# Optimization experiments

Measured on AMD Instinct MI355X. Metric: run time of the kernel, lower is better.

The kernel has to match this reference:

```python
import jax, jax.numpy as jnp
import numpy as np

# Module constants (match init_kwargs / DCNv4 defaults)
N, C, H, W = 4, 256, 128, 128
G = 4                       # DCNv4 default group
KS = 3                      # kernel_size
K = KS * KS                 # 9 sampling points per group
Cg = C // G                 # channels per group
PAD_OFF = int(np.ceil(G * K * 3 / 8) * 8)  # 112, padded offset_mask dim
EPS = 1e-5                  # BatchNorm2d eps


def setup_inputs() -> dict:
    key = jax.random.key(0)
    ks = jax.random.split(key, 6)
    s = 0.05
    return {
        "x": jax.random.normal(ks[0], (N, C, H, W), jnp.float32),
        "conv_w": jax.random.normal(ks[1], (C, C, 1, 1), jnp.float32) * s,
        "bn1_gamma": jnp.ones((C,), jnp.float32),
        "bn1_beta": jnp.zeros((C,), jnp.float32),
        "bn1_mean": jnp.zeros((C,), jnp.float32),
        "bn1_var": jnp.ones((C,), jnp.float32),
        "value_w": jax.random.normal(ks[2], (C, C), jnp.float32) * s,
        "value_b": jnp.zeros((C,), jnp.float32),
        "offset_w": jax.random.normal(ks[3], (PAD_OFF, C), jnp.float32) * s,
        "offset_b": jnp.zeros((PAD_OFF,), jnp.float32),
        "out_w": jax.random.normal(ks[4], (C, C), jnp.float32) * s,
        "out_b": jnp.zeros((C,), jnp.float32),
        "bn2_gamma": jnp.ones((C,), jnp.float32),
        "bn2_beta": jnp.zeros((C,), jnp.float32),
        "bn2_mean": jnp.zeros((C,), jnp.float32),
        "bn2_var": jnp.ones((C,), jnp.float32),
    }


def _bilinear(v, lh, lw):
    """Bilinear sample v:(N,H,W,G,Cg) at float locs lh/lw:(N,H,W,G); zero outside."""
    n, h, w, g, c = v.shape
    h0 = jnp.floor(lh)
    w0 = jnp.floor(lw)
    dh = lh - h0
    dw = lw - w0
    h0i = h0.astype(jnp.int32)
    w0i = w0.astype(jnp.int32)
    vf = v.reshape(n, h * w, g, c)

    def gather(hh, ww):
        valid = (hh >= 0) & (hh < h) & (ww >= 0) & (ww < w)
        idx = jnp.clip(hh, 0, h - 1) * w + jnp.clip(ww, 0, w - 1)
        out = jnp.take_along_axis(vf, idx.reshape(n, h * w, g)[..., None], axis=1)
        return out.reshape(n, h, w, g, c) * valid[..., None].astype(v.dtype)

    w00 = (1 - dh) * (1 - dw)
    w01 = (1 - dh) * dw
    w10 = dh * (1 - dw)
    w11 = dh * dw
    return (gather(h0i, w0i) * w00[..., None]
            + gather(h0i, w0i + 1) * w01[..., None]
            + gather(h0i + 1, w0i) * w10[..., None]
            + gather(h0i + 1, w0i + 1) * w11[..., None])


def _bn(x_nchw, gamma, beta, mean, var):
    scale = (gamma / jnp.sqrt(var + EPS))[None, :, None, None]
    return x_nchw * scale + (beta - mean * gamma / jnp.sqrt(var + EPS))[None, :, None, None]


def reference(x, conv_w, bn1_gamma, bn1_beta, bn1_mean, bn1_var,
              value_w, value_b, offset_w, offset_b, out_w, out_b,
              bn2_gamma, bn2_beta, bn2_mean, bn2_var):
    n, _, h, w = x.shape
    # ---- Conv(c1,c2,k=1): 1x1 conv (no bias) + BN + SiLU ----
    y = jnp.einsum('nchw,oc->nohw', x, conv_w[:, :, 0, 0])
    y = jax.nn.silu(_bn(y, bn1_gamma, bn1_beta, bn1_mean, bn1_var))

    # ---- DCNv4 on (N, L, C) tokens ----
    t = y.transpose(0, 2, 3, 1)                      # (N,H,W,C)
    v = t @ value_w.T + value_b                      # value_proj
    om = t @ offset_w.T + offset_b                   # (N,H,W,112)
    om = om[..., : G * K * 3].reshape(n, h, w, G, K * 3)
    off = om[..., : 2 * K].reshape(n, h, w, G, K, 2) # (dx, dy) per point
    mask = om[..., 2 * K:]                           # (N,H,W,G,K), no softmax in v4
    v = v.reshape(n, h, w, G, Cg)

    hi = jnp.arange(h, dtype=jnp.float32)[None, :, None, None]
    wi = jnp.arange(w, dtype=jnp.float32)[None, None, :, None]
    out = jnp.zeros_like(v)
    for k in range(K):  # fixed small kernel loop (9 points)
        i, j = divmod(k, KS)
        lh = hi + (i - 1) + off[..., k, 1]           # stride=1, pad=1, dil=1
        lw = wi + (j - 1) + off[..., k, 0]           # offset_scale=1.0
        out = out + mask[..., k, None] * _bilinear(v, lh, lw)

    o = out.reshape(n, h, w, C) @ out_w.T + out_b    # output_proj
    o = o.transpose(0, 3, 1, 2)                      # back to NCHW

    # ---- final BN + SiLU ----
    return jax.nn.silu(_bn(o, bn2_gamma, bn2_beta, bn2_mean, bn2_var))
```

## Files before the change

### kernel.cpp

```cpp
#include <hip/hip_runtime.h>
#include <cstdint>

typedef unsigned short u16;
typedef unsigned int   u32;
typedef __attribute__((ext_vector_type(8))) __bf16 bf16x8;
typedef __attribute__((ext_vector_type(2))) float  f32x2;
typedef __attribute__((ext_vector_type(4))) float  f32x4;
typedef __attribute__((ext_vector_type(4))) u32    u32x4;

#define N_IMG 4
#define C_DIM 256
#define H_DIM 128
#define W_DIM 128
#define HW    (H_DIM * W_DIM)
#define M_TOT (N_IMG * HW)
#define CG    64
#define PADOFF 112
#define NCAT  368
#define EPSV  1e-5f

__device__ __forceinline__ u16 f2b(float f) {
  u32 u = __float_as_uint(f);
  u += 0x7fffu + ((u >> 16) & 1u);
  return (u16)(u >> 16);
}

__device__ __forceinline__ void async_cp16(const void* g, void* l) {
  __builtin_amdgcn_global_load_lds(
      (const __attribute__((address_space(1))) void*)g,
      (__attribute__((address_space(3))) void*)l, 16, 0, 0);
}

__global__ __launch_bounds__(256) void cast_all(
    const float* __restrict__ a0, u16* __restrict__ o0,
    const float* __restrict__ a1, u16* __restrict__ o1,
    const float* __restrict__ a2, u16* __restrict__ o2,
    const float* __restrict__ a3, u16* __restrict__ o3) {
  int i = blockIdx.x * 256 + threadIdx.x;
  const float* in; u16* out; int base;
  if (i < 16384)      { in = a0; out = o0; base = 0; }
  else if (i < 32768) { in = a1; out = o1; base = 16384; }
  else if (i < 39936) { in = a2; out = o2; base = 32768; }
  else                { in = a3; out = o3; base = 39936; }
  int j = i - base;
  f32x4 v = reinterpret_cast<const f32x4*>(in)[j];
  u32 lo = (u32)f2b(v[0]) | ((u32)f2b(v[1]) << 16);
  u32 hi = (u32)f2b(v[2]) | ((u32)f2b(v[3]) << 16);
  reinterpret_cast<u32*>(out)[2 * j]     = lo;
  reinterpret_cast<u32*>(out)[2 * j + 1] = hi;
}

__global__ __launch_bounds__(256, 2) void fused_proj(
    const float* __restrict__ X, const u16* __restrict__ Bc,
    const u16* __restrict__ Wcat,
    u16* __restrict__ Vv, float* __restrict__ Om,
    const float* __restrict__ vbias, const float* __restrict__ obias,
    const float* __restrict__ gamma, const float* __restrict__ beta,
    const float* __restrict__ mean, const float* __restrict__ var) {
  constexpr int BM = 128, BK = 32;
  __shared__ __align__(16) u16 T[BM * C_DIM];
  __shared__ __align__(16) u16 As[BM * BK];
  __shared__ __align__(16) u16 Bs[BM * BK];
  const int tid  = threadIdx.x;
  const int lane = tid & 63;
  const int wave = tid >> 6;
  const int quad = lane >> 4;
  const int l16  = lane & 15;
  const int bm = blockIdx.x * BM;
  const int wm = (wave & 1) * 64;
  const int wn = (wave >> 1) * 64;
  const int img = bm >> 14;
  const int hw0 = bm & (HW - 1);
  const int p2  = (tid & 63) * 2;
  const int hh  = tid >> 6;
  const float* xb = X + (size_t)img * C_DIM * HW + hw0 + p2;

  f32x4 acc0[4][4] = {};
  f32x4 acc1[4][4] = {};
  for (int ko = 0; ko < C_DIM; ko += BK) {
    float a0[8], a1[8];
#pragma unroll
    for (int j = 0; j < 8; ++j) {
      f32x2 fv = *reinterpret_cast<const f32x2*>(
          xb + (size_t)(ko + hh * 8 + j) * HW);
      a0[j] = fv.x; a1[j] = fv.y;
    }
    u32x4 w0, w1;
#pragma unroll
    for (int j = 0; j < 4; ++j) {
      w0[j] = (u32)f2b(a0[2 * j]) | ((u32)f2b(a0[2 * j + 1]) << 16);
      w1[j] = (u32)f2b(a1[2 * j]) | ((u32)f2b(a1[2 * j + 1]) << 16);
    }
    {
      u32x4* Ar = reinterpret_cast<u32x4*>(As);
      int sw = hh ^ ((p2 >> 1) & 3);
      Ar[p2 * 4 + sw]       = w0;
      Ar[(p2 + 1) * 4 + sw] = w1;
    }
#pragma unroll
    for (int it = 0; it < 2; ++it) {
      int chunk = it * 256 + tid;
      int r  = chunk >> 2;
      int kk = (chunk & 3) << 3;
      async_cp16(Bc + (size_t)r * C_DIM + (ko + kk),
                 Bs + (size_t)(it * 256 + wave * 64) * 8);
    }
    __syncthreads();
    const bf16x8* Apf = reinterpret_cast<const bf16x8*>(As);
    const bf16x8* Bpf = reinterpret_cast<const bf16x8*>(Bs);
    bf16x8 af[4];
#pragma unroll
    for (int mi = 0; mi < 4; ++mi) {
      int r = wm + mi * 16 + l16;
      af[mi] = Apf[r * 4 + (quad ^ ((r >> 1) & 3))];
    }
    {
      bf16x8 bfr[4];
#pragma unroll
      for (int ni = 0; ni < 4; ++ni)
        bfr[ni] = Bpf[(wn + ni * 16 + l16) * 4 + quad];
#pragma unroll
      for (int mi = 0; mi < 4; ++mi)
#pragma unroll
        for (int ni = 0; ni < 4; ++ni)
          acc0[mi][ni] = __builtin_amdgcn_mfma_f32_16x16x32_bf16(
              af[mi], bfr[ni], acc0[mi][ni], 0, 0, 0);
    }
    __syncthreads();
#pragma unroll
    for (int it = 0; it < 2; ++it) {
      int chunk = it * 256 + tid;
      int r  = chunk >> 2;
      int kk = (chunk & 3) << 3;
      async_cp16(Bc + (size_t)(128 + r) * C_DIM + (ko + kk),
                 Bs + (size_t)(it * 256 + wave * 64) * 8);
    }
    __syncthreads();
    {
      bf16x8 bfr[4];
#pragma unroll
      for (int ni = 0; ni < 4; ++ni)
        bfr[ni] = Bpf[(wn + ni * 16 + l16) * 4 + quad];
#pragma unroll
      for (int mi = 0; mi < 4; ++mi)
#pragma unroll
        for (int ni = 0; ni < 4; ++ni)
          acc1[mi][ni] = __builtin_amdgcn_mfma_f32_16x16x32_bf16(
              af[mi], bfr[ni], acc1[mi][ni], 0, 0, 0);
    }
    __syncthreads();
  }
  auto epi1 = [&](f32x4 (&acc)[4][4], int bn) {
#pragma unroll
    for (int ni = 0; ni < 4; ++ni) {
      int n = bn + wn + ni * 16 + l16;
      float sc = gamma[n] * rsqrtf(var[n] + EPSV);
      float sh = beta[n] - mean[n] * sc;
#pragma unroll
      for (int mi = 0; mi < 4; ++mi) {
        int row = wm + mi * 16 + quad * 4;
#pragma unroll
        for (int i = 0; i < 4; ++i) {
          float y = acc[mi][ni][i] * sc + sh;
          y = y / (1.f + __expf(-y));
          int rr = row + i;
          T[rr * C_DIM + (((n >> 3) ^ (rr & 15)) << 3) + (n & 7)] = f2b(y);
        }
      }
    }
  };
  epi1(acc0, 0);
  epi1(acc1, 128);
  __syncthreads();

  auto stage2 = [&](u16* buf, int n0, int ko) {
#pragma unroll
    for (int it = 0; it < 2; ++it) {
      int chunk = it * 256 + tid;
      int r  = chunk >> 2;
      int kk = (chunk & 3) << 3;
      int br = n0 + r; if (br >= NCAT) br = NCAT - 1;
      async_cp16(Wcat + (size_t)br * C_DIM + (ko + kk),
                 buf + (size_t)(it * 256 + wave * 64) * 8);
    }
  };
  for (int nc = 0; nc < 3; ++nc) {
    const int n0 = nc * 128;
    f32x4 acc[4][4] = {};
    stage2(As, n0, 0);
    for (int koi = 0; koi < 8; ++koi) {
      const u16* cur = (koi & 1) ? Bs : As;
      u16*       nxt = (koi & 1) ? As : Bs;
      if (koi < 7) {
        stage2(nxt, n0, (koi + 1) * BK);
        asm volatile("s_waitcnt vmcnt(2)" ::: "memory");
      } else {
        asm volatile("s_waitcnt vmcnt(0)" ::: "memory");
      }
      __builtin_amdgcn_sched_barrier(0);
      __builtin_amdgcn_s_barrier();
      __builtin_amdgcn_sched_barrier(0);
      const bf16x8* Bpf = reinterpret_cast<const bf16x8*>(cur);
      bf16x8 af[4], bfr[4];
#pragma unroll
      for (int mi = 0; mi < 4; ++mi) {
        int row = wm + mi * 16 + l16;
        int ch  = koi * 4 + quad;
        af[mi] = *reinterpret_cast<const bf16x8*>(
            &T[row * C_DIM + ((ch ^ (row & 15)) << 3)]);
      }
#pragma unroll
      for (int ni = 0; ni < 4; ++ni)
        bfr[ni] = Bpf[(wn + ni * 16 + l16) * 4 + quad];
#pragma unroll
      for (int mi = 0; mi < 4; ++mi)
#pragma unroll
        for (int ni = 0; ni < 4; ++ni)
          acc[mi][ni] = __builtin_amdgcn_mfma_f32_16x16x32_bf16(
              af[mi], bfr[ni], acc[mi][ni], 0, 0, 0);
      __builtin_amdgcn_sched_barrier(0);
      __builtin_amdgcn_s_barrier();
    }
#pragma unroll
    for (int ni = 0; ni < 4; ++ni) {
      int n = n0 + wn + ni * 16 + l16;
      if (n < C_DIM) {
        float sh = vbias[n];
#pragma unroll
        for (int mi = 0; mi < 4; ++mi) {
          int mrow = bm + wm + mi * 16 + quad * 4;
#pragma unroll
          for (int i = 0; i < 4; ++i)
            Vv[(size_t)(mrow + i) * C_DIM + n] = f2b(acc[mi][ni][i] + sh);
        }
      } else {
        int col = n - C_DIM;
        bool ok = col < PADOFF;
        float sh = ok ? obias[col] : 0.f;
#pragma unroll
        for (int mi = 0; mi < 4; ++mi) {
          int mrow = bm + wm + mi * 16 + quad * 4;
#pragma unroll
          for (int i = 0; i < 4; ++i)
            if (ok) Om[(size_t)(mrow + i) * PADOFF + col] = acc[mi][ni][i] + sh;
        }
      }
    }
  }
}

__global__ __launch_bounds__(256) void gemm_out(
    const u16* __restrict__ A, const u16* __restrict__ B,
    float* __restrict__ Cf,
    const float* __restrict__ bias,
    const float* __restrict__ gamma, const float* __restrict__ beta,
    const float* __restrict__ mean, const float* __restrict__ var) {
  constexpr int BM = 128, BK = 32;
  __shared__ __align__(16) u16 As[2][BM * BK];
  __shared__ __align__(16) u16 Bs[2][BM * BK];
  const int tid  = threadIdx.x;
  const int lane = tid & 63;
  const int wave = tid >> 6;
  const int quad = lane >> 4;
  const int l16  = lane & 15;
  const int bm = blockIdx.x * BM;
  const int bn = blockIdx.y * BM;
  const int wm = (wave & 1) * 64;
  const int wn = (wave >> 1) * 64;

  auto stage = [&](int buf, int ko) {
#pragma unroll
    for (int it = 0; it < 2; ++it) {
      int chunk = it * 256 + tid;
      int r  = chunk >> 2;
      int kk = (chunk & 3) << 3;
      async_cp16(A + (size_t)(bm + r) * C_DIM + (ko + kk),
                 &As[buf][(it * 256 + wave * 64) * 8]);
      async_cp16(B + (size_t)(bn + r) * C_DIM + (ko + kk),
                 &Bs[buf][(it * 256 + wave * 64) * 8]);
    }
  };

  f32x4 acc[4][4] = {};

  stage(0, 0);
  for (int t = 0; t < 8; ++t) {
    const int cur = t & 1;
    if (t < 7) {
      stage(cur ^ 1, (t + 1) * BK);
      asm volatile("s_waitcnt vmcnt(4)" ::: "memory");
    } else {
      asm volatile("s_waitcnt vmcnt(0)" ::: "memory");
    }
    __builtin_amdgcn_sched_barrier(0);
    __builtin_amdgcn_s_barrier();
    __builtin_amdgcn_sched_barrier(0);
    const bf16x8* Ap = reinterpret_cast<const bf16x8*>(As[cur]);
    const bf16x8* Bp = reinterpret_cast<const bf16x8*>(Bs[cur]);
    bf16x8 af[4], bfr[4];
#pragma unroll
    for (int mi = 0; mi < 4; ++mi) af[mi] = Ap[(wm + mi * 16 + l16) * 4 + quad];
#pragma unroll
    for (int ni = 0; ni < 4; ++ni) bfr[ni] = Bp[(wn + ni * 16 + l16) * 4 + quad];
#pragma unroll
    for (int mi = 0; mi < 4; ++mi)
#pragma unroll
      for (int ni = 0; ni < 4; ++ni)
        acc[mi][ni] = __builtin_amdgcn_mfma_f32_16x16x32_bf16(
            af[mi], bfr[ni], acc[mi][ni], 0, 0, 0);
    __builtin_amdgcn_sched_barrier(0);
    __builtin_amdgcn_s_barrier();
  }

#pragma unroll
  for (int ni = 0; ni < 4; ++ni) {
    int n = bn + wn + ni * 16 + l16;
    float sc = gamma[n] * rsqrtf(var[n] + EPSV);
    float sh = beta[n] - mean[n] * sc + bias[n] * sc;
#pragma unroll
    for (int mi = 0; mi < 4; ++mi) {
      int mrow = bm + wm + mi * 16 + quad * 4;
      int img = mrow >> 14;
      int hw  = mrow & (HW - 1);
      f32x4 y;
#pragma unroll
      for (int i = 0; i < 4; ++i) {
        float z = acc[mi][ni][i] * sc + sh;
        y[i] = z / (1.f + __expf(-z));
      }
      *reinterpret_cast<f32x4*>(
          Cf + (size_t)img * C_DIM * HW + (size_t)n * HW + hw) = y;
    }
  }
}

__global__ __launch_bounds__(256) void dcn_sample(
    const u16* __restrict__ v, const float* __restrict__ om,
    u16* __restrict__ outp) {
  __shared__ float sm[16 * PADOFF];
  const int tid = threadIdx.x;
  const int bid = blockIdx.x;
  const int cpx = gridDim.x >> 3;
  const int wg  = (bid & 7) * cpx + (bid >> 3);
  const int m0  = wg * 16;
  {
    const float* src = om + (size_t)m0 * PADOFF;
#pragma unroll
    for (int i = 0; i < 7; ++i) sm[tid + i * 256] = src[tid + i * 256];
  }
  __syncthreads();
  const int c4 = tid & 3;
  const int g  = (tid >> 2) & 3;
  const int pl = tid >> 4;
  const int m  = m0 + pl;
  const int n  = m >> 14;
  const int hw = m & (HW - 1);
  const int h = hw >> 7, w = hw & 127;
  const float* p = sm + pl * PADOFF + g * 27;
  const u16* vb = v + (size_t)n * HW * C_DIM + g * CG + c4 * 16;
  float acc[16] = {};
#pragma unroll
  for (int k = 0; k < 9; ++k) {
    const int di = k / 3 - 1, dj = k % 3 - 1;
    float ox = p[2 * k], oy = p[2 * k + 1], mk = p[18 + k];
    float lh = (float)(h + di) + oy;
    float lw = (float)(w + dj) + ox;
    float fh = floorf(lh), fw = floorf(lw);
    float dh = lh - fh, dw = lw - fw;
    int h0 = (int)fh, w0 = (int)fw;
    float wy0 = (1.f - dh) * mk, wy1 = dh * mk;
    float wx0 = 1.f - dw, wx1 = dw;
    bool okw0 = (u32)w0 < (u32)W_DIM;
    bool okw1 = (u32)(w0 + 1) < (u32)W_DIM;
    int w0c = min(max(w0, 0), W_DIM - 1);
    int w1c = min(max(w0 + 1, 0), W_DIM - 1);
#pragma unroll
    for (int cy = 0; cy < 2; ++cy) {
      int hh = h0 + cy;
      bool okh = (u32)hh < (u32)H_DIM;
      int hc = min(max(hh, 0), H_DIM - 1);
      const u16* rowp = vb + (size_t)(hc << 7) * C_DIM;
      const u16* qA = rowp + (size_t)w0c * C_DIM;
      const u16* qB = rowp + (size_t)w1c * C_DIM;
      u32x4 a0 = *reinterpret_cast<const u32x4*>(qA);
      u32x4 a1 = *reinterpret_cast<const u32x4*>(qA + 8);
      u32x4 b0 = *reinterpret_cast<const u32x4*>(qB);
      u32x4 b1 = *reinterpret_cast<const u32x4*>(qB + 8);
      float wyc = (cy == 0) ? wy0 : wy1;
      float wtA = (okh && okw0) ? wyc * wx0 : 0.f;
      float wtB = (okh && okw1) ? wyc * wx1 : 0.f;
      u32 wp;
      asm("v_cvt_pk_bf16_f32 %0, %1, %2" : "=v"(wp) : "v"(wtA), "v"(wtB));
#pragma unroll
      for (int j = 0; j < 4; ++j) {
        u32 lo0 = __builtin_amdgcn_perm(a0[j], b0[j], 0x01000504u);
        u32 hi0 = __builtin_amdgcn_perm(a0[j], b0[j], 0x03020706u);
        u32 lo1 = __builtin_amdgcn_perm(a1[j], b1[j], 0x01000504u);
        u32 hi1 = __builtin_amdgcn_perm(a1[j], b1[j], 0x03020706u);
        asm("v_dot2_f32_bf16 %0, %1, %2, %3"
            : "=v"(acc[2 * j]) : "v"(lo0), "v"(wp), "v"(acc[2 * j]));
        asm("v_dot2_f32_bf16 %0, %1, %2, %3"
            : "=v"(acc[2 * j + 1]) : "v"(hi0), "v"(wp), "v"(acc[2 * j + 1]));
        asm("v_dot2_f32_bf16 %0, %1, %2, %3"
            : "=v"(acc[8 + 2 * j]) : "v"(lo1), "v"(wp), "v"(acc[8 + 2 * j]));
        asm("v_dot2_f32_bf16 %0, %1, %2, %3"
            : "=v"(acc[8 + 2 * j + 1]) : "v"(hi1), "v"(wp), "v"(acc[8 + 2 * j + 1]));
      }
    }
  }
  u32x4 r0, r1;
#pragma unroll
  for (int j = 0; j < 4; ++j) {
    u32 pa, pb;
    asm("v_cvt_pk_bf16_f32 %0, %1, %2"
        : "=v"(pa) : "v"(acc[2 * j]), "v"(acc[2 * j + 1]));
    asm("v_cvt_pk_bf16_f32 %0, %1, %2"
        : "=v"(pb) : "v"(acc[8 + 2 * j]), "v"(acc[8 + 2 * j + 1]));
    r0[j] = pa; r1[j] = pb;
  }
  u16* o = outp + (size_t)m * C_DIM + g * CG + c4 * 16;
  *reinterpret_cast<u32x4*>(o)     = r0;
  *reinterpret_cast<u32x4*>(o + 8) = r1;
}

extern "C" void kernel_launch(void* const* d_in, const int* in_sizes, int n_in,
                              void* d_out, int out_size, void* d_ws, size_t ws_size,
                              hipStream_t stream) {
  const float* x        = (const float*)d_in[0];
  const float* conv_w   = (const float*)d_in[1];
  const float* bn1_g    = (const float*)d_in[2];
  const float* bn1_b    = (const float*)d_in[3];
  const float* bn1_m    = (const float*)d_in[4];
  const float* bn1_v    = (const float*)d_in[5];
  const float* value_w  = (const float*)d_in[6];
  const float* value_b  = (const float*)d_in[7];
  const float* offset_w = (const float*)d_in[8];
  const float* offset_b = (const float*)d_in[9];
  const float* out_w    = (const float*)d_in[10];
  const float* out_b    = (const float*)d_in[11];
  const float* bn2_g    = (const float*)d_in[12];
  const float* bn2_b    = (const float*)d_in[13];
  const float* bn2_m    = (const float*)d_in[14];
  const float* bn2_v    = (const float*)d_in[15];

  char* ws = (char*)d_ws;
  u16*   vv   = (u16*)(ws);
  float* om   = (float*)(ws + 33554432);
  u16*   dcn  = (u16*)(ws + 67108864);
  u16*   wc   = (u16*)(ws + 100663296);
  u16*   wcat = (u16*)(ws + 100794368);
  u16*   wout = (u16*)(ws + 100982784);
  float* outp = (float*)d_out;

  cast_all<<<220, 256, 0, stream>>>(conv_w, wc, value_w, wcat,
                                    offset_w, wcat + 65536, out_w, wout);

  fused_proj<<<dim3(M_TOT / 128), 256, 0, stream>>>(
      x, wc, wcat, vv, om, value_b, offset_b,
      bn1_g, bn1_b, bn1_m, bn1_v);
  dcn_sample<<<dim3(M_TOT / 16), 256, 0, stream>>>(vv, om, dcn);
  gemm_out<<<dim3(M_TOT / 128, 2), 256, 0, stream>>>(
      dcn, wout, outp, out_b, bn2_g, bn2_b, bn2_m, bn2_v);
}
```

Baseline: 252.0 us.

## Double-buffer A and B tiles in first GEMM to overlap loads with MFMA

Restructures the first conv GEMM's K loop into a software pipeline. The next A tile (fp32 x converted to bf16) and the next B half-tile are prefetched into second buffers carved out of the unused T shared-memory region while the current MFMAs run. Explicit vmcnt waits and scheduling barriers replace the plain __syncthreads, with the goal of hiding global-load latency. In exchange it holds more registers for the prefetched values and relies on hand-counted waitcnt ordering being correct.

```diff
diff --git a/kernel.cpp b/kernel.cpp
--- a/kernel.cpp
+++ b/kernel.cpp
@@ -75,80 +75,98 @@
   const int hh  = tid >> 6;
   const float* xb = X + (size_t)img * C_DIM * HW + hw0 + p2;
 
-  f32x4 acc0[4][4] = {};
-  f32x4 acc1[4][4] = {};
-  for (int ko = 0; ko < C_DIM; ko += BK) {
-    float a0[8], a1[8];
-#pragma unroll
-    for (int j = 0; j < 8; ++j) {
-      f32x2 fv = *reinterpret_cast<const f32x2*>(
-          xb + (size_t)(ko + hh * 8 + j) * HW);
-      a0[j] = fv.x; a1[j] = fv.y;
-    }
-    u32x4 w0, w1;
-#pragma unroll
-    for (int j = 0; j < 4; ++j) {
-      w0[j] = (u32)f2b(a0[2 * j]) | ((u32)f2b(a0[2 * j + 1]) << 16);
-      w1[j] = (u32)f2b(a1[2 * j]) | ((u32)f2b(a1[2 * j + 1]) << 16);
-    }
-    {
-      u32x4* Ar = reinterpret_cast<u32x4*>(As);
-      int sw = hh ^ ((p2 >> 1) & 3);
-      Ar[p2 * 4 + sw]       = w0;
-      Ar[(p2 + 1) * 4 + sw] = w1;
-    }
+  u16* A1 = T;
+  u16* B1 = T + 4096;
+
+  auto issueB = [&](int s, u16* buf) {
+    int h = s & 1, ko2 = s >> 1;
 #pragma unroll
     for (int it = 0; it < 2; ++it) {
       int chunk = it * 256 + tid;
       int r  = chunk >> 2;
       int kk = (chunk & 3) << 3;
-      async_cp16(Bc + (size_t)r * C_DIM + (ko + kk),
-                 Bs + (size_t)(it * 256 + wave * 64) * 8);
-    }
-    __syncthreads();
-    const bf16x8* Apf = reinterpret_cast<const bf16x8*>(As);
-    const bf16x8* Bpf = reinterpret_cast<const bf16x8*>(Bs);
-    bf16x8 af[4];
+      async_cp16(Bc + (size_t)(h * 128 + r) * C_DIM + (ko2 * 32 + kk),
+                 buf + (size_t)(it * 256 + wave * 64) * 8);
+    }
+  };
+  auto writeA = [&](const f32x2 (&xv)[8], u16* dst) {
+    u32x4 w0, w1;
+#pragma unroll
+    for (int j = 0; j < 4; ++j) {
+      w0[j] = (u32)f2b(xv[2 * j].x) | ((u32)f2b(xv[2 * j + 1].x) << 16);
+      w1[j] = (u32)f2b(xv[2 * j].y) | ((u32)f2b(xv[2 * j + 1].y) << 16);
+    }
+    u32x4* Ar = reinterpret_cast<u32x4*>(dst);
+    int sw = hh ^ ((p2 >> 1) & 3);
+    Ar[p2 * 4 + sw]       = w0;
+    Ar[(p2 + 1) * 4 + sw] = w1;
+  };
+  auto mfma_half = [&](const u16* Abuf, const u16* Bbuf, f32x4 (&acc)[4][4]) {
+    const bf16x8* Apf = reinterpret_cast<const bf16x8*>(Abuf);
+    const bf16x8* Bpf = reinterpret_cast<const bf16x8*>(Bbuf);
+    bf16x8 af[4], bfr[4];
 #pragma unroll
     for (int mi = 0; mi < 4; ++mi) {
       int r = wm + mi * 16 + l16;
       af[mi] = Apf[r * 4 + (quad ^ ((r >> 1) & 3))];
     }
-    {
-      bf16x8 bfr[4];
+#pragma unroll
+    for (int ni = 0; ni < 4; ++ni)
+      bfr[ni] = Bpf[(wn + ni * 16 + l16) * 4 + quad];
+#pragma unroll
+    for (int mi = 0; mi < 4; ++mi)
 #pragma unroll
       for (int ni = 0; ni < 4; ++ni)
-        bfr[ni] = Bpf[(wn + ni * 16 + l16) * 4 + quad];
-#pragma unroll
-      for (int mi = 0; mi < 4; ++mi)
-#pragma unroll
-        for (int ni = 0; ni < 4; ++ni)
-          acc0[mi][ni] = __builtin_amdgcn_mfma_f32_16x16x32_bf16(
-              af[mi], bfr[ni], acc0[mi][ni], 0, 0, 0);
-    }
+        acc[mi][ni] = __builtin_amdgcn_mfma_f32_16x16x32_bf16(
+            af[mi], bfr[ni], acc[mi][ni], 0, 0, 0);
+  };
+
+  f32x4 acc0[4][4] = {};
+  f32x4 acc1[4][4] = {};
+  {
+    f32x2 xv[8];
+#pragma unroll
+    for (int j = 0; j < 8; ++j)
+      xv[j] = *reinterpret_cast<const f32x2*>(xb + (size_t)(hh * 8 + j) * HW);
+    issueB(0, Bs);
+    writeA(xv, As);
     __syncthreads();
-#pragma unroll
-    for (int it = 0; it < 2; ++it) {
-      int chunk = it * 256 + tid;
-      int r  = chunk >> 2;
-      int kk = (chunk & 3) << 3;
-      async_cp16(Bc + (size_t)(128 + r) * C_DIM + (ko + kk),
-                 Bs + (size_t)(it * 256 + wave * 64) * 8);
-    }
-    __syncthreads();
-    {
-      bf16x8 bfr[4];
-#pragma unroll
-      for (int ni = 0; ni < 4; ++ni)
-        bfr[ni] = Bpf[(wn + ni * 16 + l16) * 4 + quad];
-#pragma unroll
-      for (int mi = 0; mi < 4; ++mi)
-#pragma unroll
-        for (int ni = 0; ni < 4; ++ni)
-          acc1[mi][ni] = __builtin_amdgcn_mfma_f32_16x16x32_bf16(
-              af[mi], bfr[ni], acc1[mi][ni], 0, 0, 0);
-    }
-    __syncthreads();
+  }
+  for (int ko = 0; ko < 8; ++ko) {
+    u16* Acur = (ko & 1) ? A1 : As;
+    u16* Anxt = (ko & 1) ? As : A1;
+    f32x2 xv[8];
+    const bool haveA = (ko < 7);
+    if (haveA) {
+#pragma unroll
+      for (int j = 0; j < 8; ++j)
+        xv[j] = *reinterpret_cast<const f32x2*>(
+            xb + (size_t)((ko + 1) * 32 + hh * 8 + j) * HW);
+    }
+    __builtin_amdgcn_sched_barrier(0);
+    issueB(2 * ko + 1, B1);
+    if (haveA) writeA(xv, Anxt);
+    asm volatile("s_waitcnt vmcnt(2) lgkmcnt(0)" ::: "memory");
+    __builtin_amdgcn_sched_barrier(0);
+    __builtin_amdgcn_s_barrier();
+    __builtin_amdgcn_sched_barrier(0);
+    mfma_half(Acur, Bs, acc0);
+    __builtin_amdgcn_sched_barrier(0);
+    __builtin_amdgcn_s_barrier();
+    __builtin_amdgcn_sched_barrier(0);
+    if (ko < 7) {
+      issueB(2 * ko + 2, Bs);
+      asm volatile("s_waitcnt vmcnt(2)" ::: "memory");
+    } else {
+      asm volatile("s_waitcnt vmcnt(0)" ::: "memory");
+    }
+    __builtin_amdgcn_sched_barrier(0);
+    __builtin_amdgcn_s_barrier();
+    __builtin_amdgcn_sched_barrier(0);
+    mfma_half(Acur, B1, acc1);
+    __builtin_amdgcn_sched_barrier(0);
+    __builtin_amdgcn_s_barrier();
+    __builtin_amdgcn_sched_barrier(0);
   }
   auto epi1 = [&](f32x4 (&acc)[4][4], int bn) {
 #pragma unroll
```

Measured after the change: 251.2 us. Within noise of the previous version (-0.3%).
